# Optimization experiments

Measured on AMD Instinct MI355X. Metric: run time of the kernel, lower is better.

## Reference

```python
import jax, jax.numpy as jnp
import numpy as np

N = 512          # number of gaussians
H = 256
W = 256
TANX = 0.5
TANY = 0.5
FX = W / (2.0 * TANX)   # focal_x
FY = H / (2.0 * TANY)   # focal_y


def setup_inputs() -> dict:
    key = jax.random.key(0)
    k = jax.random.split(key, 6)
    xy = (jax.random.uniform(k[0], (N, 2)) - 0.5) * 4.0
    z = jax.random.uniform(k[1], (N, 1)) * 4.0 + 2.0   # in front of camera
    means3D = jnp.concatenate([xy, z], axis=1)
    means2D = jnp.zeros((N, 3), jnp.float32)            # gradient holder in torch; unused in math
    opacities = jax.random.uniform(k[2], (N, 1)) * 0.9 + 0.05
    colors_precomp = jax.random.uniform(k[3], (N, 3))
    scales = jax.random.uniform(k[4], (N, 3)) * 0.08 + 0.02
    rotations = jax.random.normal(k[5], (N, 4))         # normalized inside kernel, as in CUDA
    viewmatrix = jnp.eye(4, dtype=jnp.float32)
    znear, zfar = 0.01, 100.0
    proj = jnp.array([[1.0 / TANX, 0, 0, 0],
                      [0, 1.0 / TANY, 0, 0],
                      [0, 0, zfar / (zfar - znear), -(zfar * znear) / (zfar - znear)],
                      [0, 0, 1.0, 0]], dtype=jnp.float32)
    projmatrix = proj @ viewmatrix
    bg = jnp.zeros((3,), jnp.float32)
    return {"means3D": means3D, "means2D": means2D, "opacities": opacities,
            "colors_precomp": colors_precomp, "scales": scales, "rotations": rotations,
            "viewmatrix": viewmatrix, "projmatrix": projmatrix, "bg": bg}


def _forward(means3D, opacities, colors_precomp, scales, rotations, viewmatrix, projmatrix, bg):
    dt = means3D.dtype
    # --- 3D covariance from scale/rotation (computeCov3D) ---
    q = rotations / jnp.linalg.norm(rotations, axis=1, keepdims=True)
    r, x, y, z = q[:, 0], q[:, 1], q[:, 2], q[:, 3]
    R = jnp.stack([
        jnp.stack([1 - 2 * (y * y + z * z), 2 * (x * y - r * z), 2 * (x * z + r * y)], -1),
        jnp.stack([2 * (x * y + r * z), 1 - 2 * (x * x + z * z), 2 * (y * z - r * x)], -1),
        jnp.stack([2 * (x * z - r * y), 2 * (y * z + r * x), 1 - 2 * (x * x + y * y)], -1)], -2)
    Sigma = jnp.einsum('nij,nj,nkj->nik', R, scales * scales, R)   # [N,3,3]

    # --- project to camera / screen ---
    hom = jnp.concatenate([means3D, jnp.ones((means3D.shape[0], 1), dt)], 1)
    p_view = hom @ viewmatrix.T                                    # [N,4]
    tz = p_view[:, 2]
    limx, limy = 1.3 * TANX, 1.3 * TANY
    tx = jnp.clip(p_view[:, 0] / tz, -limx, limx) * tz
    ty = jnp.clip(p_view[:, 1] / tz, -limy, limy) * tz

    # --- EWA splat: cov2D = J W Sigma W^T J^T + 0.3 I ---
    zeros = jnp.zeros_like(tz)
    J = jnp.stack([jnp.stack([FX / tz, zeros, -FX * tx / (tz * tz)], -1),
                   jnp.stack([zeros, FY / tz, -FY * ty / (tz * tz)], -1)], -2)  # [N,2,3]
    Tm = jnp.einsum('nij,jk->nik', J, viewmatrix[:3, :3])
    cov2d = jnp.einsum('nij,njk,nlk->nil', Tm, Sigma, Tm)
    a = cov2d[:, 0, 0] + 0.3
    b = cov2d[:, 0, 1]
    c = cov2d[:, 1, 1] + 0.3
    det = a * c - b * b
    inv_det = 1.0 / det
    conA, conB, conC = c * inv_det, -b * inv_det, a * inv_det

    p_hom = hom @ projmatrix.T
    pw = 1.0 / (p_hom[:, 3] + 1e-7)
    pix_x = ((p_hom[:, 0] * pw + 1.0) * W - 1.0) * 0.5
    pix_y = ((p_hom[:, 1] * pw + 1.0) * H - 1.0) * 0.5

    mid = 0.5 * (a + c)
    lam = mid + jnp.sqrt(jnp.maximum(0.1, mid * mid - det))
    valid = (tz > 0.2) & (det > 0)
    radii = (jnp.ceil(3.0 * jnp.sqrt(lam)) * valid).astype(jnp.int32)

    # --- per-pixel gaussian alpha ---
    px = jnp.arange(W, dtype=dt)
    py = jnp.arange(H, dtype=dt)
    dx = pix_x[:, None, None] - px[None, None, :]   # [N,1,W]
    dy = pix_y[:, None, None] - py[None, :, None]   # [N,H,1]
    power = (-0.5 * (conA[:, None, None] * dx * dx + conC[:, None, None] * dy * dy)
             - conB[:, None, None] * dx * dy)        # [N,H,W]
    alpha = jnp.minimum(0.99, opacities[:, :, None] * jnp.exp(power))
    alpha = jnp.where((power > 0) | (alpha < 1.0 / 255.0) | (~valid[:, None, None]), 0.0, alpha)

    # --- depth sort + front-to-back alpha compositing ---
    order = jnp.argsort(tz)
    alpha_s = alpha[order]
    col_s = colors_precomp[order]
    T_inc = jnp.cumprod(1.0 - alpha_s, axis=0)                         # transmittance after each splat
    T_excl = jnp.concatenate([jnp.ones((1, H, W), dt), T_inc[:-1]], 0)  # before each splat
    wgt = alpha_s * T_excl * (T_inc >= 1e-4)                           # CUDA early-stop at T < 1e-4
    img = jnp.einsum('nhw,nc->chw', wgt, col_s) + T_inc[-1][None] * bg[:, None, None]
    return img, radii


def reference(means3D, means2D, opacities, colors_precomp, scales, rotations, viewmatrix, projmatrix, bg):
    return _forward(means3D, opacities, colors_precomp, scales, rotations, viewmatrix, projmatrix, bg)
```

## Files before the change

kernel.cpp:

```cpp
#include <hip/hip_runtime.h>
#include <hip/hip_fp16.h>
#include <math.h>

#define N_G    512
#define IMG_H  256
#define IMG_W  256

__global__ __launch_bounds__(64) void gs_prep(
    const float* __restrict__ means3D,
    const float* __restrict__ opacities,
    const float* __restrict__ colors,
    const float* __restrict__ scales,
    const float* __restrict__ rotations,
    const float* __restrict__ viewmatrix,
    const float* __restrict__ projmatrix,
    float4* __restrict__ Gs,
    float4* __restrict__ Ga,
    float2* __restrict__ Gb,
    float* __restrict__ radii_out)
{
    const int g = blockIdx.x * 64 + threadIdx.x;

    float VM[16], PM[16];
    #pragma unroll
    for (int i = 0; i < 16; ++i) { VM[i] = viewmatrix[i]; PM[i] = projmatrix[i]; }

    const float mx = means3D[g*3+0], my = means3D[g*3+1], mz = means3D[g*3+2];
    float rq = rotations[g*4+0], xq = rotations[g*4+1], yq = rotations[g*4+2], zq = rotations[g*4+3];
    const float qn = sqrtf(rq*rq + xq*xq + yq*yq + zq*zq);
    rq /= qn; xq /= qn; yq /= qn; zq /= qn;
    const float R00 = 1.f - 2.f*(yq*yq + zq*zq);
    const float R01 = 2.f*(xq*yq - rq*zq);
    const float R02 = 2.f*(xq*zq + rq*yq);
    const float R10 = 2.f*(xq*yq + rq*zq);
    const float R11 = 1.f - 2.f*(xq*xq + zq*zq);
    const float R12 = 2.f*(yq*zq - rq*xq);
    const float R20 = 2.f*(xq*zq - rq*yq);
    const float R21 = 2.f*(yq*zq + rq*xq);
    const float R22 = 1.f - 2.f*(xq*xq + yq*yq);
    float s0 = scales[g*3+0], s1 = scales[g*3+1], s2 = scales[g*3+2];
    s0 *= s0; s1 *= s1; s2 *= s2;
    const float S00 = R00*R00*s0 + R01*R01*s1 + R02*R02*s2;
    const float S01 = R00*R10*s0 + R01*R11*s1 + R02*R12*s2;
    const float S02 = R00*R20*s0 + R01*R21*s1 + R02*R22*s2;
    const float S11 = R10*R10*s0 + R11*R11*s1 + R12*R12*s2;
    const float S12 = R10*R20*s0 + R11*R21*s1 + R12*R22*s2;
    const float S22 = R20*R20*s0 + R21*R21*s1 + R22*R22*s2;

    const float pv0 = VM[0]*mx + VM[1]*my + VM[2]*mz  + VM[3];
    const float pv1 = VM[4]*mx + VM[5]*my + VM[6]*mz  + VM[7];
    const float tz  = VM[8]*mx + VM[9]*my + VM[10]*mz + VM[11];
    const float FX = 256.f, FY = 256.f, limx = 0.65f, limy = 0.65f;
    const float tx = fminf(fmaxf(pv0/tz, -limx), limx) * tz;
    const float ty = fminf(fmaxf(pv1/tz, -limy), limy) * tz;
    const float itz = 1.f / tz, itz2 = itz*itz;
    const float J00 = FX*itz, J02 = -FX*tx*itz2;
    const float J11 = FY*itz, J12 = -FY*ty*itz2;
    const float T00 = J00*VM[0] + J02*VM[8];
    const float T01 = J00*VM[1] + J02*VM[9];
    const float T02 = J00*VM[2] + J02*VM[10];
    const float T10 = J11*VM[4] + J12*VM[8];
    const float T11 = J11*VM[5] + J12*VM[9];
    const float T12 = J11*VM[6] + J12*VM[10];
    const float u0 = T00*S00 + T01*S01 + T02*S02;
    const float u1 = T00*S01 + T01*S11 + T02*S12;
    const float u2 = T00*S02 + T01*S12 + T02*S22;
    const float v0 = T10*S00 + T11*S01 + T12*S02;
    const float v1 = T10*S01 + T11*S11 + T12*S12;
    const float v2 = T10*S02 + T11*S12 + T12*S22;
    const float c00 = u0*T00 + u1*T01 + u2*T02;
    const float c01 = u0*T10 + u1*T11 + u2*T12;
    const float c11 = v0*T10 + v1*T11 + v2*T12;
    const float a = c00 + 0.3f, b = c01, c = c11 + 0.3f;
    const float det = a*c - b*b;
    const float inv_det = 1.f/det;
    float conA = c*inv_det, conB = -b*inv_det, conC = a*inv_det;
    const float ph0 = PM[0]*mx  + PM[1]*my  + PM[2]*mz  + PM[3];
    const float ph1 = PM[4]*mx  + PM[5]*my  + PM[6]*mz  + PM[7];
    const float ph3 = PM[12]*mx + PM[13]*my + PM[14]*mz + PM[15];
    const float pw = 1.f/(ph3 + 1e-7f);
    const float pix_x = ((ph0*pw + 1.f)*(float)IMG_W - 1.f)*0.5f;
    const float pix_y = ((ph1*pw + 1.f)*(float)IMG_H - 1.f)*0.5f;
    const float mid = 0.5f*(a + c);
    const float lam = mid + sqrtf(fmaxf(0.1f, mid*mid - det));
    const bool valid = (tz > 0.2f) && (det > 0.f);
    float op = opacities[g];
    if (!valid) { conA = conB = conC = 0.f; op = 0.f; }

    radii_out[g] = valid ? ceilf(3.f*sqrtf(lam)) : 0.f;

    float rad = -1.f;
    if (valid && op * 255.f > 1.f) {
        const float r = sqrtf(2.f * lam * logf(255.f * op)) + 0.01f;
        if (pix_x + r >= 0.f && pix_x - r <= (float)(IMG_W-1) &&
            pix_y + r >= 0.f && pix_y - r <= (float)(IMG_H-1))
            rad = r;
    }

    const float lnop = logf(op);
    const float rg = __builtin_bit_cast(float, __floats2half2_rn(colors[g*3+0], colors[g*3+1]));
    Gs[g] = make_float4(pix_x, pix_y, rad, tz);
    Ga[g] = make_float4(-0.5f*conA, -conB, -0.5f*conC, lnop);
    Gb[g] = make_float2(rg, colors[g*3+2]);
}

__global__ __launch_bounds__(128) void gs_raster(
    const float4* __restrict__ Gs,
    const float4* __restrict__ Ga,
    const float2* __restrict__ Gb,
    const float* __restrict__ bg,
    float* __restrict__ img)
{
    __shared__ int    s_n;
    __shared__ float  s_tz[N_G];
    __shared__ int    s_id[N_G];
    __shared__ float2 uP[N_G];
    __shared__ float4 uA[N_G];
    __shared__ float2 uC[N_G];
    __shared__ float2 oP[N_G];
    __shared__ float4 oA[N_G];
    __shared__ float2 oC[N_G];

    const int tid = threadIdx.x;
    const int bx = blockIdx.x & 15, by = blockIdx.x >> 4;
    const float x0 = (float)(bx * 16), x1 = x0 + 15.f;
    const float y0 = (float)(by * 8),  y1 = y0 + 7.f;

    if (tid == 0) s_n = 0;

    float4 s[4], a[4];
    float2 c[4];
    #pragma unroll
    for (int k = 0; k < 4; ++k) {
        const int g = k * 128 + tid;
        s[k] = Gs[g];
        a[k] = Ga[g];
        c[k] = Gb[g];
    }
    __syncthreads();

    #pragma unroll
    for (int k = 0; k < 4; ++k) {
        const bool hit = (s[k].z > 0.f &&
                          s[k].x + s[k].z >= x0 && s[k].x - s[k].z <= x1 &&
                          s[k].y + s[k].z >= y0 && s[k].y - s[k].z <= y1);
        if (hit) {
            const int p = atomicAdd(&s_n, 1);
            s_tz[p] = s[k].w;
            s_id[p] = k * 128 + tid;
            uP[p] = make_float2(s[k].x, s[k].y);
            uA[p] = a[k];
            uC[p] = c[k];
        }
    }
    __syncthreads();

    const int nc  = s_n;
    const int ncp = (nc + 7) & ~7;

    for (int i = tid; i < nc; i += 128) {
        const float tz = s_tz[i];
        const int   id = s_id[i];
        int r = 0;
        for (int j = 0; j < nc; ++j) {
            const float tj = s_tz[j];
            r += (tj < tz) || (tj == tz && s_id[j] < id);
        }
        oP[r] = uP[i];
        oA[r] = uA[i];
        oC[r] = uC[i];
    }
    for (int i = nc + tid; i < ncp; i += 128) {
        oP[i] = make_float2(0.f, 0.f);
        oA[i] = make_float4(0.f, 0.f, 0.f, -1e30f);
        oC[i] = make_float2(0.f, 0.f);
    }
    __syncthreads();

    const int px = bx * 16 + (tid & 15), py = by * 8 + (tid >> 4);
    const float fx = (float)px, fy = (float)py;

    float T = 1.f, cr = 0.f, cg = 0.f, cb = 0.f;
    bool done = false;
    for (int base = 0; base < ncp; base += 8) {
        #pragma unroll
        for (int u = 0; u < 8; ++u) {
            const int i = base + u;
            const float2 pP = oP[i];
            const float4 pA = oA[i];
            const float2 pC = oC[i];
            const float dx = pP.x - fx;
            const float dy = pP.y - fy;
            const float power = pA.x*dx*dx + pA.y*dx*dy + pA.z*dy*dy;
            const float al = fminf(0.99f, __expf(power + pA.w));
            if (!done && !(power > 0.f || al < (1.0f/255.0f))) {
                const float Tnew = T * (1.f - al);
                if (Tnew < 1e-4f) { T = Tnew; done = true; }
                else {
                    const float wgt = al * T;
                    const float2 rg = __half22float2(__builtin_bit_cast(__half2, pC.x));
                    cr += wgt * rg.x;
                    cg += wgt * rg.y;
                    cb += wgt * pC.y;
                    T = Tnew;
                }
            }
        }
        if (__all(done)) break;
    }
    const int pix = py * IMG_W + px;
    img[pix]                   = cr + T * bg[0];
    img[IMG_H*IMG_W   + pix]   = cg + T * bg[1];
    img[2*IMG_H*IMG_W + pix]   = cb + T * bg[2];
}

extern "C" void kernel_launch(void* const* d_in, const int* in_sizes, int n_in,
                              void* d_out, int out_size, void* d_ws, size_t ws_size,
                              hipStream_t stream) {
    const float* means3D    = (const float*)d_in[0];
    const float* opacities  = (const float*)d_in[2];
    const float* colors     = (const float*)d_in[3];
    const float* scales     = (const float*)d_in[4];
    const float* rotations  = (const float*)d_in[5];
    const float* viewmatrix = (const float*)d_in[6];
    const float* projmatrix = (const float*)d_in[7];
    const float* bg         = (const float*)d_in[8];

    float* img   = (float*)d_out;
    float* radii = (float*)d_out + 3*IMG_H*IMG_W;
    float4* Gs   = (float4*)d_ws;
    float4* Ga   = Gs + N_G;
    float2* Gb   = (float2*)(Ga + N_G);

    gs_prep<<<8, 64, 0, stream>>>(means3D, opacities, colors, scales,
                                  rotations, viewmatrix, projmatrix,
                                  Gs, Ga, Gb, radii);
    gs_raster<<<(IMG_W/16)*(IMG_H/8), 128, 0, stream>>>(Gs, Ga, Gb, bg, img);
}
```

Baseline: 19.27 us.

## Fuse prep and raster kernels with a global flag spin-wait

Merges the preprocessing and rasterization kernels into one launch. The first four blocks compute per-gaussian parameters and signal a global counter, and every block spin-waits on that counter before rasterizing. The depth-rank sort is also reworked: each thread ranks its own register-held candidates against a compact key array, so the staged per-candidate shared arrays go away. This removes one kernel launch gap but adds a hipMemsetAsync, spin-wait latency, and a deadlock risk if the producer blocks are not co-resident with the waiting blocks.

Measured after the change: 57.77 us. +199.8%, slower.

```diff
diff --git a/kernel.cpp b/kernel.cpp
--- a/kernel.cpp
+++ b/kernel.cpp
@@ -6,7 +6,7 @@
 #define IMG_H  256
 #define IMG_W  256
 
-__global__ __launch_bounds__(64) void gs_prep(
+__global__ __launch_bounds__(128) void gs_all(
     const float* __restrict__ means3D,
     const float* __restrict__ opacities,
     const float* __restrict__ colors,
@@ -14,119 +14,122 @@
     const float* __restrict__ rotations,
     const float* __restrict__ viewmatrix,
     const float* __restrict__ projmatrix,
+    const float* __restrict__ bg,
     float4* __restrict__ Gs,
     float4* __restrict__ Ga,
     float2* __restrict__ Gb,
+    unsigned* __restrict__ flag,
+    float* __restrict__ img,
     float* __restrict__ radii_out)
 {
-    const int g = blockIdx.x * 64 + threadIdx.x;
-
-    float VM[16], PM[16];
-    #pragma unroll
-    for (int i = 0; i < 16; ++i) { VM[i] = viewmatrix[i]; PM[i] = projmatrix[i]; }
-
-    const float mx = means3D[g*3+0], my = means3D[g*3+1], mz = means3D[g*3+2];
-    float rq = rotations[g*4+0], xq = rotations[g*4+1], yq = rotations[g*4+2], zq = rotations[g*4+3];
-    const float qn = sqrtf(rq*rq + xq*xq + yq*yq + zq*zq);
-    rq /= qn; xq /= qn; yq /= qn; zq /= qn;
-    const float R00 = 1.f - 2.f*(yq*yq + zq*zq);
-    const float R01 = 2.f*(xq*yq - rq*zq);
-    const float R02 = 2.f*(xq*zq + rq*yq);
-    const float R10 = 2.f*(xq*yq + rq*zq);
-    const float R11 = 1.f - 2.f*(xq*xq + zq*zq);
-    const float R12 = 2.f*(yq*zq - rq*xq);
-    const float R20 = 2.f*(xq*zq - rq*yq);
-    const float R21 = 2.f*(yq*zq + rq*xq);
-    const float R22 = 1.f - 2.f*(xq*xq + yq*yq);
-    float s0 = scales[g*3+0], s1 = scales[g*3+1], s2 = scales[g*3+2];
-    s0 *= s0; s1 *= s1; s2 *= s2;
-    const float S00 = R00*R00*s0 + R01*R01*s1 + R02*R02*s2;
-    const float S01 = R00*R10*s0 + R01*R11*s1 + R02*R12*s2;
-    const float S02 = R00*R20*s0 + R01*R21*s1 + R02*R22*s2;
-    const float S11 = R10*R10*s0 + R11*R11*s1 + R12*R12*s2;
-    const float S12 = R10*R20*s0 + R11*R21*s1 + R12*R22*s2;
-    const float S22 = R20*R20*s0 + R21*R21*s1 + R22*R22*s2;
-
-    const float pv0 = VM[0]*mx + VM[1]*my + VM[2]*mz  + VM[3];
-    const float pv1 = VM[4]*mx + VM[5]*my + VM[6]*mz  + VM[7];
-    const float tz  = VM[8]*mx + VM[9]*my + VM[10]*mz + VM[11];
-    const float FX = 256.f, FY = 256.f, limx = 0.65f, limy = 0.65f;
-    const float tx = fminf(fmaxf(pv0/tz, -limx), limx) * tz;
-    const float ty = fminf(fmaxf(pv1/tz, -limy), limy) * tz;
-    const float itz = 1.f / tz, itz2 = itz*itz;
-    const float J00 = FX*itz, J02 = -FX*tx*itz2;
-    const float J11 = FY*itz, J12 = -FY*ty*itz2;
-    const float T00 = J00*VM[0] + J02*VM[8];
-    const float T01 = J00*VM[1] + J02*VM[9];
-    const float T02 = J00*VM[2] + J02*VM[10];
-    const float T10 = J11*VM[4] + J12*VM[8];
-    const float T11 = J11*VM[5] + J12*VM[9];
-    const float T12 = J11*VM[6] + J12*VM[10];
-    const float u0 = T00*S00 + T01*S01 + T02*S02;
-    const float u1 = T00*S01 + T01*S11 + T02*S12;
-    const float u2 = T00*S02 + T01*S12 + T02*S22;
-    const float v0 = T10*S00 + T11*S01 + T12*S02;
-    const float v1 = T10*S01 + T11*S11 + T12*S12;
-    const float v2 = T10*S02 + T11*S12 + T12*S22;
-    const float c00 = u0*T00 + u1*T01 + u2*T02;
-    const float c01 = u0*T10 + u1*T11 + u2*T12;
-    const float c11 = v0*T10 + v1*T11 + v2*T12;
-    const float a = c00 + 0.3f, b = c01, c = c11 + 0.3f;
-    const float det = a*c - b*b;
-    const float inv_det = 1.f/det;
-    float conA = c*inv_det, conB = -b*inv_det, conC = a*inv_det;
-    const float ph0 = PM[0]*mx  + PM[1]*my  + PM[2]*mz  + PM[3];
-    const float ph1 = PM[4]*mx  + PM[5]*my  + PM[6]*mz  + PM[7];
-    const float ph3 = PM[12]*mx + PM[13]*my + PM[14]*mz + PM[15];
-    const float pw = 1.f/(ph3 + 1e-7f);
-    const float pix_x = ((ph0*pw + 1.f)*(float)IMG_W - 1.f)*0.5f;
-    const float pix_y = ((ph1*pw + 1.f)*(float)IMG_H - 1.f)*0.5f;
-    const float mid = 0.5f*(a + c);
-    const float lam = mid + sqrtf(fmaxf(0.1f, mid*mid - det));
-    const bool valid = (tz > 0.2f) && (det > 0.f);
-    float op = opacities[g];
-    if (!valid) { conA = conB = conC = 0.f; op = 0.f; }
-
-    radii_out[g] = valid ? ceilf(3.f*sqrtf(lam)) : 0.f;
-
-    float rad = -1.f;
-    if (valid && op * 255.f > 1.f) {
-        const float r = sqrtf(2.f * lam * logf(255.f * op)) + 0.01f;
-        if (pix_x + r >= 0.f && pix_x - r <= (float)(IMG_W-1) &&
-            pix_y + r >= 0.f && pix_y - r <= (float)(IMG_H-1))
-            rad = r;
-    }
-
-    const float lnop = logf(op);
-    const float rg = __builtin_bit_cast(float, __floats2half2_rn(colors[g*3+0], colors[g*3+1]));
-    Gs[g] = make_float4(pix_x, pix_y, rad, tz);
-    Ga[g] = make_float4(-0.5f*conA, -conB, -0.5f*conC, lnop);
-    Gb[g] = make_float2(rg, colors[g*3+2]);
-}
-
-__global__ __launch_bounds__(128) void gs_raster(
-    const float4* __restrict__ Gs,
-    const float4* __restrict__ Ga,
-    const float2* __restrict__ Gb,
-    const float* __restrict__ bg,
-    float* __restrict__ img)
-{
     __shared__ int    s_n;
-    __shared__ float  s_tz[N_G];
-    __shared__ int    s_id[N_G];
-    __shared__ float2 uP[N_G];
-    __shared__ float4 uA[N_G];
-    __shared__ float2 uC[N_G];
+    __shared__ float2 s_key[N_G];
     __shared__ float2 oP[N_G];
     __shared__ float4 oA[N_G];
     __shared__ float2 oC[N_G];
 
     const int tid = threadIdx.x;
-    const int bx = blockIdx.x & 15, by = blockIdx.x >> 4;
+    const int bid = blockIdx.x;
+    if (tid == 0) s_n = 0;
+
+    if (bid < 4) {
+        const int g = bid * 128 + tid;
+        float VM[16], PM[16];
+        #pragma unroll
+        for (int i = 0; i < 16; ++i) { VM[i] = viewmatrix[i]; PM[i] = projmatrix[i]; }
+
+        const float mx = means3D[g*3+0], my = means3D[g*3+1], mz = means3D[g*3+2];
+        float rq = rotations[g*4+0], xq = rotations[g*4+1], yq = rotations[g*4+2], zq = rotations[g*4+3];
+        const float qn = sqrtf(rq*rq + xq*xq + yq*yq + zq*zq);
+        rq /= qn; xq /= qn; yq /= qn; zq /= qn;
+        const float R00 = 1.f - 2.f*(yq*yq + zq*zq);
+        const float R01 = 2.f*(xq*yq - rq*zq);
+        const float R02 = 2.f*(xq*zq + rq*yq);
+        const float R10 = 2.f*(xq*yq + rq*zq);
+        const float R11 = 1.f - 2.f*(xq*xq + zq*zq);
+        const float R12 = 2.f*(yq*zq - rq*xq);
+        const float R20 = 2.f*(xq*zq - rq*yq);
+        const float R21 = 2.f*(yq*zq + rq*xq);
+        const float R22 = 1.f - 2.f*(xq*xq + yq*yq);
+        float s0 = scales[g*3+0], s1 = scales[g*3+1], s2 = scales[g*3+2];
+        s0 *= s0; s1 *= s1; s2 *= s2;
+        const float S00 = R00*R00*s0 + R01*R01*s1 + R02*R02*s2;
+        const float S01 = R00*R10*s0 + R01*R11*s1 + R02*R12*s2;
+        const float S02 = R00*R20*s0 + R01*R21*s1 + R02*R22*s2;
+        const float S11 = R10*R10*s0 + R11*R11*s1 + R12*R12*s2;
+        const float S12 = R10*R20*s0 + R11*R21*s1 + R12*R22*s2;
+        const float S22 = R20*R20*s0 + R21*R21*s1 + R22*R22*s2;
+
+        const float pv0 = VM[0]*mx + VM[1]*my + VM[2]*mz  + VM[3];
+        const float pv1 = VM[4]*mx + VM[5]*my + VM[6]*mz  + VM[7];
+        const float tz  = VM[8]*mx + VM[9]*my + VM[10]*mz + VM[11];
+        const float FX = 256.f, FY = 256.f, limx = 0.65f, limy = 0.65f;
+        const float tx = fminf(fmaxf(pv0/tz, -limx), limx) * tz;
+        const float ty = fminf(fmaxf(pv1/tz, -limy), limy) * tz;
+        const float itz = 1.f / tz, itz2 = itz*itz;
+        const float J00 = FX*itz, J02 = -FX*tx*itz2;
+        const float J11 = FY*itz, J12 = -FY*ty*itz2;
+        const float T00 = J00*VM[0] + J02*VM[8];
+        const float T01 = J00*VM[1] + J02*VM[9];
+        const float T02 = J00*VM[2] + J02*VM[10];
+        const float T10 = J11*VM[4] + J12*VM[8];
+        const float T11 = J11*VM[5] + J12*VM[9];
+        const float T12 = J11*VM[6] + J12*VM[10];
+        const float u0 = T00*S00 + T01*S01 + T02*S02;
+        const float u1 = T00*S01 + T01*S11 + T02*S12;
+        const float u2 = T00*S02 + T01*S12 + T02*S22;
+        const float v0 = T10*S00 + T11*S01 + T12*S02;
+        const float v1 = T10*S01 + T11*S11 + T12*S12;
+        const float v2 = T10*S02 + T11*S12 + T12*S22;
+        const float c00 = u0*T00 + u1*T01 + u2*T02;
+        const float c01 = u0*T10 + u1*T11 + u2*T12;
+        const float c11 = v0*T10 + v1*T11 + v2*T12;
+        const float a = c00 + 0.3f, b = c01, c = c11 + 0.3f;
+        const float det = a*c - b*b;
+        const float inv_det = 1.f/det;
+        float conA = c*inv_det, conB = -b*inv_det, conC = a*inv_det;
+        const float ph0 = PM[0]*mx  + PM[1]*my  + PM[2]*mz  + PM[3];
+        const float ph1 = PM[4]*mx  + PM[5]*my  + PM[6]*mz  + PM[7];
+        const float ph3 = PM[12]*mx + PM[13]*my + PM[14]*mz + PM[15];
+        const float pw = 1.f/(ph3 + 1e-7f);
+        const float pix_x = ((ph0*pw + 1.f)*(float)IMG_W - 1.f)*0.5f;
+        const float pix_y = ((ph1*pw + 1.f)*(float)IMG_H - 1.f)*0.5f;
+        const float mid = 0.5f*(a + c);
+        const float lam = mid + sqrtf(fmaxf(0.1f, mid*mid - det));
+        const bool valid = (tz > 0.2f) && (det > 0.f);
+        float op = opacities[g];
+        if (!valid) { conA = conB = conC = 0.f; op = 0.f; }
+
+        radii_out[g] = valid ? ceilf(3.f*sqrtf(lam)) : 0.f;
+
+        float rad = -1.f;
+        if (valid && op * 255.f > 1.f) {
+            const float r = sqrtf(2.f * lam * logf(255.f * op)) + 0.01f;
+            if (pix_x + r >= 0.f && pix_x - r <= (float)(IMG_W-1) &&
+                pix_y + r >= 0.f && pix_y - r <= (float)(IMG_H-1))
+                rad = r;
+        }
+
+        const float lnop = logf(op);
+        const float rg = __builtin_bit_cast(float, __floats2half2_rn(colors[g*3+0], colors[g*3+1]));
+        Gs[g] = make_float4(pix_x, pix_y, rad, tz);
+        Ga[g] = make_float4(-0.5f*conA, -conB, -0.5f*conC, lnop);
+        Gb[g] = make_float2(rg, colors[g*3+2]);
+
+        __syncthreads();
+        if (tid == 0) {
+            __threadfence();
+            __hip_atomic_fetch_add(flag, 1u, __ATOMIC_RELEASE, __HIP_MEMORY_SCOPE_AGENT);
+        }
+    }
+
+    while (__hip_atomic_load(flag, __ATOMIC_ACQUIRE, __HIP_MEMORY_SCOPE_AGENT) < 4u)
+        __builtin_amdgcn_s_sleep(2);
+    __syncthreads();
+
+    const int bx = bid & 15, by = bid >> 4;
     const float x0 = (float)(bx * 16), x1 = x0 + 15.f;
     const float y0 = (float)(by * 8),  y1 = y0 + 7.f;
-
-    if (tid == 0) s_n = 0;
 
     float4 s[4], a[4];
     float2 c[4];
@@ -137,20 +140,16 @@
         a[k] = Ga[g];
         c[k] = Gb[g];
     }
-    __syncthreads();
-
+
+    bool hit[4];
     #pragma unroll
     for (int k = 0; k < 4; ++k) {
-        const bool hit = (s[k].z > 0.f &&
-                          s[k].x + s[k].z >= x0 && s[k].x - s[k].z <= x1 &&
-                          s[k].y + s[k].z >= y0 && s[k].y - s[k].z <= y1);
-        if (hit) {
+        hit[k] = (s[k].z > 0.f &&
+                  s[k].x + s[k].z >= x0 && s[k].x - s[k].z <= x1 &&
+                  s[k].y + s[k].z >= y0 && s[k].y - s[k].z <= y1);
+        if (hit[k]) {
             const int p = atomicAdd(&s_n, 1);
-            s_tz[p] = s[k].w;
-            s_id[p] = k * 128 + tid;
-            uP[p] = make_float2(s[k].x, s[k].y);
-            uA[p] = a[k];
-            uC[p] = c[k];
+            s_key[p] = make_float2(s[k].w, __int_as_float(k * 128 + tid));
         }
     }
     __syncthreads();
@@ -158,17 +157,23 @@
     const int nc  = s_n;
     const int ncp = (nc + 7) & ~7;
 
-    for (int i = tid; i < nc; i += 128) {
-        const float tz = s_tz[i];
-        const int   id = s_id[i];
-        int r = 0;
+    if (hit[0] | hit[1] | hit[2] | hit[3]) {
+        int r[4] = {0, 0, 0, 0};
         for (int j = 0; j < nc; ++j) {
-            const float tj = s_tz[j];
-            r += (tj < tz) || (tj == tz && s_id[j] < id);
-        }
-        oP[r] = uP[i];
-        oA[r] = uA[i];
-        oC[r] = uC[i];
+            const float2 kj = s_key[j];
+            const int  idj = __float_as_int(kj.y);
+            #pragma unroll
+            for (int k = 0; k < 4; ++k)
+                r[k] += (kj.x < s[k].w) || (kj.x == s[k].w && idj < (k * 128 + tid));
+        }
+        #pragma unroll
+        for (int k = 0; k < 4; ++k) {
+            if (hit[k]) {
+                oP[r[k]] = make_float2(s[k].x, s[k].y);
+                oA[r[k]] = a[k];
+                oC[r[k]] = c[k];
+            }
+        }
     }
     for (int i = nc + tid; i < ncp; i += 128) {
         oP[i] = make_float2(0.f, 0.f);
@@ -231,9 +236,10 @@
     float4* Gs   = (float4*)d_ws;
     float4* Ga   = Gs + N_G;
     float2* Gb   = (float2*)(Ga + N_G);
-
-    gs_prep<<<8, 64, 0, stream>>>(means3D, opacities, colors, scales,
-                                  rotations, viewmatrix, projmatrix,
-                                  Gs, Ga, Gb, radii);
-    gs_raster<<<(IMG_W/16)*(IMG_H/8), 128, 0, stream>>>(Gs, Ga, Gb, bg, img);
+    unsigned* flag = (unsigned*)((char*)d_ws + N_G*(16+16+8));
+
+    hipMemsetAsync(flag, 0, sizeof(unsigned), stream);
+    gs_all<<<(IMG_W/16)*(IMG_H/8), 128, 0, stream>>>(
+        means3D, opacities, colors, scales, rotations,
+        viewmatrix, projmatrix, bg, Gs, Ga, Gb, flag, img, radii);
 }
```

## Shrink raster tiles to 8x8 single-wave blocks with register-resident rank sort

Applied to the files above, without the earlier changes.

Raster blocks become one 64-lane wave covering an 8x8 tile, doubling the block count. Each lane keeps its eight candidate gaussians in registers and ranks them against a compact shared key array, so the staging buffers go away and Ga/Gb are read only for hits. The conic and opacity terms are pre-scaled by log2(e) so the per-pixel exponent is a raw exp2 instruction. Smaller tiles let blocks stop early more finely but repeat the culling and sort work more times, and each block does less work overall.

Result: slower. 25.36 us (+31.6%).

```diff
diff --git a/kernel.cpp b/kernel.cpp
--- a/kernel.cpp
+++ b/kernel.cpp
@@ -97,14 +97,15 @@
             rad = r;
     }
 
-    const float lnop = logf(op);
+    const float il2 = 1.4426950408889634f;
+    const float l2op = log2f(op);
     const float rg = __builtin_bit_cast(float, __floats2half2_rn(colors[g*3+0], colors[g*3+1]));
     Gs[g] = make_float4(pix_x, pix_y, rad, tz);
-    Ga[g] = make_float4(-0.5f*conA, -conB, -0.5f*conC, lnop);
+    Ga[g] = make_float4(-0.5f*conA*il2, -conB*il2, -0.5f*conC*il2, l2op);
     Gb[g] = make_float2(rg, colors[g*3+2]);
 }
 
-__global__ __launch_bounds__(128) void gs_raster(
+__global__ __launch_bounds__(64) void gs_raster(
     const float4* __restrict__ Gs,
     const float4* __restrict__ Ga,
     const float2* __restrict__ Gb,
@@ -112,45 +113,37 @@
     float* __restrict__ img)
 {
     __shared__ int    s_n;
-    __shared__ float  s_tz[N_G];
-    __shared__ int    s_id[N_G];
-    __shared__ float2 uP[N_G];
-    __shared__ float4 uA[N_G];
-    __shared__ float2 uC[N_G];
+    __shared__ float2 s_key[N_G];
     __shared__ float2 oP[N_G];
     __shared__ float4 oA[N_G];
     __shared__ float2 oC[N_G];
 
-    const int tid = threadIdx.x;
-    const int bx = blockIdx.x & 15, by = blockIdx.x >> 4;
-    const float x0 = (float)(bx * 16), x1 = x0 + 15.f;
-    const float y0 = (float)(by * 8),  y1 = y0 + 7.f;
-
-    if (tid == 0) s_n = 0;
-
-    float4 s[4], a[4];
-    float2 c[4];
+    const int lane = threadIdx.x;
+    const int bx = blockIdx.x & 31, by = blockIdx.x >> 5;
+    const float x0 = (float)(bx * 8), x1 = x0 + 7.f;
+    const float y0 = (float)(by * 8), y1 = y0 + 7.f;
+
+    if (lane == 0) s_n = 0;
+
+    float4 s[8];
     #pragma unroll
-    for (int k = 0; k < 4; ++k) {
-        const int g = k * 128 + tid;
-        s[k] = Gs[g];
-        a[k] = Ga[g];
-        c[k] = Gb[g];
-    }
+    for (int k = 0; k < 8; ++k) s[k] = Gs[k * 64 + lane];
     __syncthreads();
 
+    bool hit[8];
+    float4 a[8];
+    float2 c[8];
     #pragma unroll
-    for (int k = 0; k < 4; ++k) {
-        const bool hit = (s[k].z > 0.f &&
-                          s[k].x + s[k].z >= x0 && s[k].x - s[k].z <= x1 &&
-                          s[k].y + s[k].z >= y0 && s[k].y - s[k].z <= y1);
-        if (hit) {
+    for (int k = 0; k < 8; ++k) {
+        hit[k] = (s[k].z > 0.f &&
+                  s[k].x + s[k].z >= x0 && s[k].x - s[k].z <= x1 &&
+                  s[k].y + s[k].z >= y0 && s[k].y - s[k].z <= y1);
+        if (hit[k]) {
+            const int g = k * 64 + lane;
             const int p = atomicAdd(&s_n, 1);
-            s_tz[p] = s[k].w;
-            s_id[p] = k * 128 + tid;
-            uP[p] = make_float2(s[k].x, s[k].y);
-            uA[p] = a[k];
-            uC[p] = c[k];
+            s_key[p] = make_float2(s[k].w, __int_as_float(g));
+            a[k] = Ga[g];
+            c[k] = Gb[g];
         }
     }
     __syncthreads();
@@ -158,26 +151,32 @@
     const int nc  = s_n;
     const int ncp = (nc + 7) & ~7;
 
-    for (int i = tid; i < nc; i += 128) {
-        const float tz = s_tz[i];
-        const int   id = s_id[i];
-        int r = 0;
+    if (hit[0] | hit[1] | hit[2] | hit[3] | hit[4] | hit[5] | hit[6] | hit[7]) {
+        int r[8] = {0,0,0,0,0,0,0,0};
         for (int j = 0; j < nc; ++j) {
-            const float tj = s_tz[j];
-            r += (tj < tz) || (tj == tz && s_id[j] < id);
-        }
-        oP[r] = uP[i];
-        oA[r] = uA[i];
-        oC[r] = uC[i];
-    }
-    for (int i = nc + tid; i < ncp; i += 128) {
+            const float2 kj = s_key[j];
+            const int  idj = __float_as_int(kj.y);
+            #pragma unroll
+            for (int k = 0; k < 8; ++k)
+                r[k] += (kj.x < s[k].w) || (kj.x == s[k].w && idj < (k * 64 + lane));
+        }
+        #pragma unroll
+        for (int k = 0; k < 8; ++k) {
+            if (hit[k]) {
+                oP[r[k]] = make_float2(s[k].x, s[k].y);
+                oA[r[k]] = a[k];
+                oC[r[k]] = c[k];
+            }
+        }
+    }
+    for (int i = nc + lane; i < ncp; i += 64) {
         oP[i] = make_float2(0.f, 0.f);
         oA[i] = make_float4(0.f, 0.f, 0.f, -1e30f);
         oC[i] = make_float2(0.f, 0.f);
     }
     __syncthreads();
 
-    const int px = bx * 16 + (tid & 15), py = by * 8 + (tid >> 4);
+    const int px = bx * 8 + (lane & 7), py = by * 8 + (lane >> 3);
     const float fx = (float)px, fy = (float)py;
 
     float T = 1.f, cr = 0.f, cg = 0.f, cb = 0.f;
@@ -192,7 +191,7 @@
             const float dx = pP.x - fx;
             const float dy = pP.y - fy;
             const float power = pA.x*dx*dx + pA.y*dx*dy + pA.z*dy*dy;
-            const float al = fminf(0.99f, __expf(power + pA.w));
+            const float al = fminf(0.99f, __builtin_amdgcn_exp2f(power + pA.w));
             if (!done && !(power > 0.f || al < (1.0f/255.0f))) {
                 const float Tnew = T * (1.f - al);
                 if (Tnew < 1e-4f) { T = Tnew; done = true; }
@@ -235,5 +234,5 @@
     gs_prep<<<8, 64, 0, stream>>>(means3D, opacities, colors, scales,
                                   rotations, viewmatrix, projmatrix,
                                   Gs, Ga, Gb, radii);
-    gs_raster<<<(IMG_W/16)*(IMG_H/8), 128, 0, stream>>>(Gs, Ga, Gb, bg, img);
+    gs_raster<<<(IMG_W/8)*(IMG_H/8), 64, 0, stream>>>(Gs, Ga, Gb, bg, img);
 }
```

## Sort gaussians globally in prep kernel and compact per tile with ballots

Applied to the files above, without the earlier changes.

The prep kernel now computes each gaussian's view depth into shared memory, ranks all gaussians by depth, and writes the outputs in sorted order. This removes the per-tile O(n^2) depth sort from the raster kernel, which now only compacts hits per tile, in order, using wave ballots and mbcnt prefix counts instead of shared atomics. The conic coefficients and log-opacity are pre-scaled by log2(e) so the raster loop can call the hardware exp2 directly. The prep kernel assumes 8 blocks of 64 threads (tid*8 covers all 512), and the shared depth must match the tz computed later for the ranking to be consistent.

After: 28.51 us. 48.0% more time.

```diff
diff --git a/kernel.cpp b/kernel.cpp
--- a/kernel.cpp
+++ b/kernel.cpp
@@ -19,11 +19,20 @@
     float2* __restrict__ Gb,
     float* __restrict__ radii_out)
 {
-    const int g = blockIdx.x * 64 + threadIdx.x;
+    __shared__ float s_tz[N_G];
+    const int tid = threadIdx.x;
+    const int g = blockIdx.x * 64 + tid;
 
     float VM[16], PM[16];
     #pragma unroll
     for (int i = 0; i < 16; ++i) { VM[i] = viewmatrix[i]; PM[i] = projmatrix[i]; }
+
+    #pragma unroll
+    for (int q = 0; q < 8; ++q) {
+        const int j = tid * 8 + q;
+        s_tz[j] = VM[8]*means3D[j*3+0] + VM[9]*means3D[j*3+1]
+                + VM[10]*means3D[j*3+2] + VM[11];
+    }
 
     const float mx = means3D[g*3+0], my = means3D[g*3+1], mz = means3D[g*3+2];
     float rq = rotations[g*4+0], xq = rotations[g*4+1], yq = rotations[g*4+2], zq = rotations[g*4+3];
@@ -97,11 +106,26 @@
             rad = r;
     }
 
-    const float lnop = logf(op);
+    __syncthreads();
+
+    int rk = 0;
+    const float4* t4 = (const float4*)s_tz;
+    #pragma unroll 8
+    for (int j4 = 0; j4 < N_G/4; ++j4) {
+        const float4 t = t4[j4];
+        const int j = j4 * 4;
+        rk += (t.x < tz) || (t.x == tz && (j+0) < g);
+        rk += (t.y < tz) || (t.y == tz && (j+1) < g);
+        rk += (t.z < tz) || (t.z == tz && (j+2) < g);
+        rk += (t.w < tz) || (t.w == tz && (j+3) < g);
+    }
+
+    const float il2 = 1.4426950408889634f;
+    const float l2op = log2f(op);
     const float rg = __builtin_bit_cast(float, __floats2half2_rn(colors[g*3+0], colors[g*3+1]));
-    Gs[g] = make_float4(pix_x, pix_y, rad, tz);
-    Ga[g] = make_float4(-0.5f*conA, -conB, -0.5f*conC, lnop);
-    Gb[g] = make_float2(rg, colors[g*3+2]);
+    Gs[rk] = make_float4(pix_x, pix_y, rad, tz);
+    Ga[rk] = make_float4(-0.5f*conA*il2, -conB*il2, -0.5f*conC*il2, l2op);
+    Gb[rk] = make_float2(rg, colors[g*3+2]);
 }
 
 __global__ __launch_bounds__(128) void gs_raster(
@@ -111,64 +135,53 @@
     const float* __restrict__ bg,
     float* __restrict__ img)
 {
-    __shared__ int    s_n;
-    __shared__ float  s_tz[N_G];
-    __shared__ int    s_id[N_G];
-    __shared__ float2 uP[N_G];
-    __shared__ float4 uA[N_G];
-    __shared__ float2 uC[N_G];
-    __shared__ float2 oP[N_G];
-    __shared__ float4 oA[N_G];
-    __shared__ float2 oC[N_G];
-
-    const int tid = threadIdx.x;
+    __shared__ int    s_wn[2];
+    __shared__ float2 oP[N_G + 8];
+    __shared__ float4 oA[N_G + 8];
+    __shared__ float2 oC[N_G + 8];
+
+    const int tid  = threadIdx.x;
+    const int w    = tid >> 6;
+    const int lane = tid & 63;
     const int bx = blockIdx.x & 15, by = blockIdx.x >> 4;
     const float x0 = (float)(bx * 16), x1 = x0 + 15.f;
     const float y0 = (float)(by * 8),  y1 = y0 + 7.f;
 
-    if (tid == 0) s_n = 0;
-
-    float4 s[4], a[4];
-    float2 c[4];
-    #pragma unroll
-    for (int k = 0; k < 4; ++k) {
-        const int g = k * 128 + tid;
-        s[k] = Gs[g];
-        a[k] = Ga[g];
-        c[k] = Gb[g];
-    }
+    float4 s[4];
+    #pragma unroll
+    for (int c = 0; c < 4; ++c) s[c] = Gs[w*256 + c*64 + lane];
+
+    bool hit[4];
+    unsigned long long msk[4];
+    int wave_cnt = 0;
+    #pragma unroll
+    for (int c = 0; c < 4; ++c) {
+        hit[c] = (s[c].z > 0.f &&
+                  s[c].x + s[c].z >= x0 && s[c].x - s[c].z <= x1 &&
+                  s[c].y + s[c].z >= y0 && s[c].y - s[c].z <= y1);
+        msk[c] = __ballot(hit[c]);
+        wave_cnt += __popcll(msk[c]);
+    }
+    if (lane == 0) s_wn[w] = wave_cnt;
     __syncthreads();
 
-    #pragma unroll
-    for (int k = 0; k < 4; ++k) {
-        const bool hit = (s[k].z > 0.f &&
-                          s[k].x + s[k].z >= x0 && s[k].x - s[k].z <= x1 &&
-                          s[k].y + s[k].z >= y0 && s[k].y - s[k].z <= y1);
-        if (hit) {
-            const int p = atomicAdd(&s_n, 1);
-            s_tz[p] = s[k].w;
-            s_id[p] = k * 128 + tid;
-            uP[p] = make_float2(s[k].x, s[k].y);
-            uA[p] = a[k];
-            uC[p] = c[k];
+    const int w0 = s_wn[0];
+    const int nc = w0 + s_wn[1];
+    const int ncp = (nc + 7) & ~7;
+    int pos = (w == 0) ? 0 : w0;
+
+    #pragma unroll
+    for (int c = 0; c < 4; ++c) {
+        if (hit[c]) {
+            const int g = w*256 + c*64 + lane;
+            const int p = pos + __builtin_amdgcn_mbcnt_hi(
+                (unsigned)(msk[c] >> 32),
+                __builtin_amdgcn_mbcnt_lo((unsigned)msk[c], 0));
+            oP[p] = make_float2(s[c].x, s[c].y);
+            oA[p] = Ga[g];
+            oC[p] = Gb[g];
         }
-    }
-    __syncthreads();
-
-    const int nc  = s_n;
-    const int ncp = (nc + 7) & ~7;
-
-    for (int i = tid; i < nc; i += 128) {
-        const float tz = s_tz[i];
-        const int   id = s_id[i];
-        int r = 0;
-        for (int j = 0; j < nc; ++j) {
-            const float tj = s_tz[j];
-            r += (tj < tz) || (tj == tz && s_id[j] < id);
-        }
-        oP[r] = uP[i];
-        oA[r] = uA[i];
-        oC[r] = uC[i];
+        pos += __popcll(msk[c]);
     }
     for (int i = nc + tid; i < ncp; i += 128) {
         oP[i] = make_float2(0.f, 0.f);
@@ -192,7 +205,7 @@
             const float dx = pP.x - fx;
             const float dy = pP.y - fy;
             const float power = pA.x*dx*dx + pA.y*dx*dy + pA.z*dy*dy;
-            const float al = fminf(0.99f, __expf(power + pA.w));
+            const float al = fminf(0.99f, __builtin_amdgcn_exp2f(power + pA.w));
             if (!done && !(power > 0.f || al < (1.0f/255.0f))) {
                 const float Tnew = T * (1.f - al);
                 if (Tnew < 1e-4f) { T = Tnew; done = true; }
```
